# Kernel optimization log

Hardware: AMD Instinct MI355X
Metric: run time of the kernel (lower is better)

The kernel has to match this reference:

```python
import jax, jax.numpy as jnp
import numpy as np

DIM = 128
HEADS = 4
HD = DIM // HEADS  # 32
WS = 8             # search window (ws x ws candidates)
K = 16             # top-k neighbors kept
SCALE = HD ** -0.5


def _sepconv(x, w_dw, w_pw, b):
    # depthwise 3x3 ('SAME', reflect-free) + pointwise 1x1 with bias (SepConv2d)
    C = x.shape[1]
    y = jax.lax.conv_general_dilated(x, w_dw, (1, 1), 'SAME',
                                     feature_group_count=C,
                                     dimension_numbers=('NCHW', 'OIHW', 'NCHW'))
    return jnp.einsum('bchw,oc->bohw', y, w_pw) + b[None, :, None, None]


def _refl(i, n):
    # dnls reflect_bounds: mirror indices back into [0, n-1]
    i = jnp.where(i < 0, -i, i)
    return jnp.where(i >= n, 2 * (n - 1) - i, i)


def _neighbor_idx(T, H, W, ws):
    # flat pixel index of the ws*ws spatial candidates per query (wt=0: same frame)
    off = jnp.arange(ws) - ws // 2
    ni = _refl(jnp.arange(H)[:, None] + off[None, :], H)  # [H,ws]
    nj = _refl(jnp.arange(W)[:, None] + off[None, :], W)  # [W,ws]
    pix = ni[:, None, :, None] * W + nj[None, :, None, :]  # [H,W,ws,ws]
    idx = jnp.arange(T)[:, None, None, None, None] * (H * W) + pix[None]
    return idx.reshape(T * H * W, ws * ws).astype(jnp.int32)  # [Q,L]


def reference(vid, wq_dw, wq_pw, bq, wk_dw, wk_pw, bk, wv_dw, wv_pw, bv, proj_w, proj_b):
    B, T, C, H, W = vid.shape
    Q = T * H * W
    x = vid.reshape(B * T, C, H, W)
    # qkv conv projection; q pre-scaled as in get_qkv
    q = _sepconv(x, wq_dw, wq_pw, bq) * SCALE
    k = _sepconv(x, wk_dw, wk_pw, bk)
    v = _sepconv(x, wv_dw, wv_pw, bv)

    def heads(z):  # [B*T,C,H,W] -> [B,heads,Q,hd]
        return z.reshape(B, T, HEADS, HD, H, W).transpose(0, 2, 1, 4, 5, 3).reshape(B, HEADS, Q, HD)

    qh, kh, vh = heads(q), heads(k), heads(v)
    idx = _neighbor_idx(T, H, W, WS)            # [Q,L]
    kg = jnp.take(kh, idx, axis=2)              # [B,h,Q,L,hd] irregular gather
    dists = jnp.einsum('bhqd,bhqld->bhql', qh, kg)
    vals, args = jax.lax.top_k(dists, K)        # k-NN by prod distance
    attn = jax.nn.softmax(vals, axis=-1)        # run_softmax over k
    sel = jnp.take_along_axis(jnp.broadcast_to(idx[None, None], (B, HEADS) + idx.shape), args, axis=-1)
    vsel = jnp.take_along_axis(vh, sel.reshape(B, HEADS, Q * K)[..., None], axis=2).reshape(B, HEADS, Q, K, HD)
    out = jnp.einsum('bhqk,bhqkd->bhqd', attn, vsel)   # wpsum (ps=pt=1)
    out = out.transpose(0, 2, 1, 3).reshape(B, Q, C)   # merge heads: (h c)
    y = out @ proj_w.T + proj_b                        # nn.Linear proj
    # fold: ps=1, stride0=1 -> zvid==1, pure reshape back to video
    return y.reshape(B, T, H, W, C).transpose(0, 1, 4, 2, 3)


def setup_inputs() -> dict:
    key = jax.random.key(0)
    ks = jax.random.split(key, 12)
    s = 0.02
    return {
        'vid': jax.random.normal(ks[0], (1, 2, DIM, 96, 96), jnp.float32),
        'wq_dw': jax.random.normal(ks[1], (DIM, 1, 3, 3), jnp.float32) * s,
        'wq_pw': jax.random.normal(ks[2], (DIM, DIM), jnp.float32) * s,
        'bq': jax.random.normal(ks[3], (DIM,), jnp.float32) * s,
        'wk_dw': jax.random.normal(ks[4], (DIM, 1, 3, 3), jnp.float32) * s,
        'wk_pw': jax.random.normal(ks[5], (DIM, DIM), jnp.float32) * s,
        'bk': jax.random.normal(ks[6], (DIM,), jnp.float32) * s,
        'wv_dw': jax.random.normal(ks[7], (DIM, 1, 3, 3), jnp.float32) * s,
        'wv_pw': jax.random.normal(ks[8], (DIM, DIM), jnp.float32) * s,
        'bv': jax.random.normal(ks[9], (DIM,), jnp.float32) * s,
        'proj_w': jax.random.normal(ks[10], (DIM, DIM), jnp.float32) * s,
        'proj_b': jax.random.normal(ks[11], (DIM,), jnp.float32) * s,
    }
```

## Files before the change

### kernel.cpp

```cpp
#include <hip/hip_runtime.h>
#include <math.h>

#define TT 2
#define CH 128
#define HH 96
#define WW 96
#define HWS 9216
#define QTOT 18432
#define QC (QTOT*CH)
#define HD 32
#define KTOP 16
#define SCALE 0.17677669529663687f

#define SEG 16
#define PR 8
#define PC 23
#define PSTRIDE 36

#define FPX 32

#define WB_TOT 98304

typedef __attribute__((ext_vector_type(8))) short short8;
typedef __attribute__((ext_vector_type(4))) float floatx4;

__device__ __forceinline__ unsigned short f2bf(float f) {
    union { float f; unsigned u; } x; x.f = f;
    unsigned r = x.u + 0x7fffu + ((x.u >> 16) & 1u);
    return (unsigned short)(r >> 16);
}
__device__ __forceinline__ float bf2f(unsigned short h) {
    return __uint_as_float(((unsigned)h) << 16);
}

__device__ __forceinline__ int refl(int x, int n) {
    x = x < 0 ? -x : x;
    return x >= n ? 2 * (n - 1) - x : x;
}

__global__ __launch_bounds__(256) void wprep_kernel(
    const float* __restrict__ wq_pw, const float* __restrict__ wk_pw,
    const float* __restrict__ wv_pw, const float* __restrict__ proj_w,
    unsigned short* __restrict__ wbuf)
{
    int t = threadIdx.x;
    int y = blockIdx.x;
    const float* src = y == 0 ? wq_pw : (y == 1 ? wk_pw : (y == 2 ? wv_pw : proj_w));
    unsigned short* hi = wbuf + (y == 0 ? 0 : (y == 1 ? 32768 : (y == 2 ? 65536 : 81920)));
#pragma unroll
    for (int r = 0; r < 16; r++) {
        int idx = r * 256 + t;
        float4 w4 = *(const float4*)(src + idx * 4);
        unsigned short hx = f2bf(w4.x), hy = f2bf(w4.y), hz = f2bf(w4.z), hw = f2bf(w4.w);
        uint2 pk;
        pk.x = hx | ((unsigned)hy << 16); pk.y = hz | ((unsigned)hw << 16);
        *(uint2*)(hi + idx * 4) = pk;
        if (y < 2) {
            unsigned short lx = f2bf(w4.x - bf2f(hx)), ly = f2bf(w4.y - bf2f(hy));
            unsigned short lz = f2bf(w4.z - bf2f(hz)), lw = f2bf(w4.w - bf2f(hw));
            pk.x = lx | ((unsigned)ly << 16); pk.y = lz | ((unsigned)lw << 16);
            *(uint2*)(hi + 16384 + idx * 4) = pk;
        }
    }
}

__global__ __launch_bounds__(512) void dwqkv_kernel(
    const float* __restrict__ x,
    const float* __restrict__ wqd, const float* __restrict__ wkd, const float* __restrict__ wvd,
    const unsigned short* __restrict__ wbuf,
    const float* __restrict__ bq, const float* __restrict__ bk, const float* __restrict__ bv,
    float* __restrict__ qkf,
    unsigned short* __restrict__ vh)
{
    __shared__ float wS[3456];
    __shared__ unsigned short pl[5][FPX * 136];
    int t = threadIdx.x;
    for (int r = t; r < 1152; r += 512) {
        wS[r] = wqd[r]; wS[1152 + r] = wkd[r]; wS[2304 + r] = wvd[r];
    }
    int p0 = blockIdx.x * FPX;
    int tt0 = p0 / HWS;
    int hw0 = p0 - tt0 * HWS;
    int i0 = hw0 / WW, j0 = hw0 - i0 * WW;
    int px = t & 31, cgp = t >> 5;
    int c0 = cgp * 8;
    int j = j0 + px;

    int off[9]; float mk[9];
#pragma unroll
    for (int r = 0; r < 3; r++) {
        int ii = i0 + r - 1;
        float rm = (ii >= 0 && ii < HH) ? 1.f : 0.f;
        int iic = ii < 0 ? 0 : (ii >= HH ? HH - 1 : ii);
#pragma unroll
        for (int s = 0; s < 3; s++) {
            int jj = j + s - 1;
            float cm = (jj >= 0 && jj < WW) ? 1.f : 0.f;
            int jjc = jj < 0 ? 0 : (jj >= WW ? WW - 1 : jj);
            off[r * 3 + s] = iic * WW + jjc;
            mk[r * 3 + s] = rm * cm;
        }
    }
    __syncthreads();

    unsigned qh[4], ql2[4], kh[4], kl[4], vh4[4];
#pragma unroll
    for (int ic = 0; ic < 8; ic += 2) {
        float sv[3][2];
#pragma unroll
        for (int u = 0; u < 2; u++) {
            int c = c0 + ic + u;
            const float* xp = x + (size_t)(tt0 * CH + c) * HWS;
            const float* w0 = &wS[c * 9];
            const float* w1 = &wS[1152 + c * 9];
            const float* w2 = &wS[2304 + c * 9];
            float s0 = 0.f, s1 = 0.f, s2 = 0.f;
#pragma unroll
            for (int q9 = 0; q9 < 9; q9++) {
                float xv = xp[off[q9]] * mk[q9];
                s0 += xv * w0[q9]; s1 += xv * w1[q9]; s2 += xv * w2[q9];
            }
            sv[0][u] = s0; sv[1][u] = s1; sv[2][u] = s2;
        }
        int w = ic >> 1;
        unsigned short h0 = f2bf(sv[0][0]), h1 = f2bf(sv[0][1]);
        qh[w] = h0 | ((unsigned)h1 << 16);
        ql2[w] = f2bf(sv[0][0] - bf2f(h0)) | ((unsigned)f2bf(sv[0][1] - bf2f(h1)) << 16);
        h0 = f2bf(sv[1][0]); h1 = f2bf(sv[1][1]);
        kh[w] = h0 | ((unsigned)h1 << 16);
        kl[w] = f2bf(sv[1][0] - bf2f(h0)) | ((unsigned)f2bf(sv[1][1] - bf2f(h1)) << 16);
        vh4[w] = f2bf(sv[2][0]) | ((unsigned)f2bf(sv[2][1]) << 16);
    }
    int lb = px * 136 + c0;
    uint4 pk;
    pk.x = qh[0];  pk.y = qh[1];  pk.z = qh[2];  pk.w = qh[3];  *(uint4*)&pl[0][lb] = pk;
    pk.x = ql2[0]; pk.y = ql2[1]; pk.z = ql2[2]; pk.w = ql2[3]; *(uint4*)&pl[1][lb] = pk;
    pk.x = kh[0];  pk.y = kh[1];  pk.z = kh[2];  pk.w = kh[3];  *(uint4*)&pl[2][lb] = pk;
    pk.x = kl[0];  pk.y = kl[1];  pk.z = kl[2];  pk.w = kl[3];  *(uint4*)&pl[3][lb] = pk;
    pk.x = vh4[0]; pk.y = vh4[1]; pk.z = vh4[2]; pk.w = vh4[3]; *(uint4*)&pl[4][lb] = pk;
    __syncthreads();

    int wv = t >> 6, lane = t & 63;
    int m = lane & 15, quad = lane >> 4;
    int o0 = (wv & 3) * 32;
    bool isQ = wv < 4;
    const unsigned short* Wh_g = wbuf + (isQ ? 0 : 32768);
    const unsigned short* Wl_g = Wh_g + 16384;
    const unsigned short* Ah = pl[isQ ? 0 : 2];
    const unsigned short* Al = pl[isQ ? 1 : 3];
    const float* bias = isQ ? bq : bk;
    float scale = isQ ? SCALE : 1.f;
    float* O = qkf + (isQ ? 0 : (size_t)QC);
    float bb[2];
#pragma unroll
    for (int ot = 0; ot < 2; ot++) bb[ot] = bias[o0 + ot * 16 + m];
    floatx4 acc[2][2];
#pragma unroll
    for (int i = 0; i < 2; i++)
#pragma unroll
        for (int jj2 = 0; jj2 < 2; jj2++) acc[i][jj2] = (floatx4){0.f, 0.f, 0.f, 0.f};
#pragma unroll
    for (int kc = 0; kc < 4; kc++) {
        short8 avh[2], avl[2], bh2[2], bl2[2];
#pragma unroll
        for (int pt = 0; pt < 2; pt++) {
            int lidx = (pt * 16 + m) * 136 + kc * 32 + quad * 8;
            avh[pt] = *(const short8*)&Ah[lidx];
            avl[pt] = *(const short8*)&Al[lidx];
        }
#pragma unroll
        for (int ot = 0; ot < 2; ot++) {
            size_t widx = (size_t)(o0 + ot * 16 + m) * CH + kc * 32 + quad * 8;
            bh2[ot] = *(const short8*)(Wh_g + widx);
            bl2[ot] = *(const short8*)(Wl_g + widx);
        }
#pragma unroll
        for (int pt = 0; pt < 2; pt++)
#pragma unroll
            for (int ot = 0; ot < 2; ot++) {
                acc[pt][ot] = __builtin_amdgcn_mfma_f32_16x16x32_bf16(avh[pt], bh2[ot], acc[pt][ot], 0, 0, 0);
                acc[pt][ot] = __builtin_amdgcn_mfma_f32_16x16x32_bf16(avh[pt], bl2[ot], acc[pt][ot], 0, 0, 0);
                acc[pt][ot] = __builtin_amdgcn_mfma_f32_16x16x32_bf16(avl[pt], bh2[ot], acc[pt][ot], 0, 0, 0);
            }
    }
#pragma unroll
    for (int pt = 0; pt < 2; pt++)
#pragma unroll
        for (int ot = 0; ot < 2; ot++)
#pragma unroll
            for (int reg = 0; reg < 4; reg++) {
                int p = p0 + pt * 16 + quad * 4 + reg;
                O[(size_t)p * CH + o0 + ot * 16 + m] = (acc[pt][ot][reg] + bb[ot]) * scale;
            }

    const unsigned short* Wv_g = wbuf + 65536;
    int ptv = wv >> 2;
    float bbv[2];
#pragma unroll
    for (int ot = 0; ot < 2; ot++) bbv[ot] = bv[o0 + ot * 16 + m];
    floatx4 accv[2];
    accv[0] = (floatx4){0.f, 0.f, 0.f, 0.f};
    accv[1] = (floatx4){0.f, 0.f, 0.f, 0.f};
#pragma unroll
    for (int kc = 0; kc < 4; kc++) {
        int lidx = (ptv * 16 + m) * 136 + kc * 32 + quad * 8;
        short8 av = *(const short8*)&pl[4][lidx];
#pragma unroll
        for (int ot = 0; ot < 2; ot++) {
            size_t widx = (size_t)(o0 + ot * 16 + m) * CH + kc * 32 + quad * 8;
            short8 bhv = *(const short8*)(Wv_g + widx);
            accv[ot] = __builtin_amdgcn_mfma_f32_16x16x32_bf16(av, bhv, accv[ot], 0, 0, 0);
        }
    }
    unsigned short* vhh = vh + (size_t)(wv & 3) * QTOT * 32;
#pragma unroll
    for (int ot = 0; ot < 2; ot++)
#pragma unroll
        for (int reg = 0; reg < 4; reg++) {
            int p = p0 + ptv * 16 + quad * 4 + reg;
            vhh[(size_t)p * 32 + ot * 16 + m] = f2bf(accv[ot][reg] + bbv[ot]);
        }
}

__global__ __launch_bounds__(1024) void attn_kernel(
    const float* __restrict__ q,
    const float* __restrict__ k,
    const unsigned short* __restrict__ vh,
    unsigned short* __restrict__ att)
{
    __shared__ float kp[PR * PC * PSTRIDE];
    __shared__ uint2 slot[16][KTOP];
    int h = blockIdx.y;
    int n = blockIdx.x;
    int seg = (n & 7) * 144 + (n >> 3);
    int qj0 = (seg % (WW / SEG)) * SEG;
    int qi = (seg / (WW / SEG)) % HH;
    int tt = seg / ((WW / SEG) * HH);
    int t = threadIdx.x;

#pragma unroll
    for (int r = 0; r < 2; r++) {
        int f = r * 1024 + t;
        if (f < PR * PC * 8) {
            int pix = f >> 3, d4 = f & 7;
            int ci = pix / PC, cj = pix - ci * PC;
            int gi = refl(qi + ci - 4, HH);
            int gj = refl(qj0 + cj - 4, WW);
            int gp = tt * HWS + gi * WW + gj;
            *(float4*)(&kp[pix * PSTRIDE + d4 * 4]) =
                *(const float4*)(k + (size_t)gp * CH + h * HD + d4 * 4);
        }
    }

    int wv = t >> 6, lane = t & 63;
    int wvu = __builtin_amdgcn_readfirstlane(wv);
    if (lane < KTOP) slot[wvu][lane] = make_uint2(0u, 0u);
    __syncthreads();

    int ci = lane >> 3, cjo = lane & 7;
    int di = ci - 4, dj = cjo - 4;
    int rowoff = tt * HWS + refl(qi + di, HH) * WW;
    const unsigned long long below = (1ull << lane) - 1ull;
    const unsigned short* vhh = vh + (size_t)h * QTOT * 32;

    int ql = wvu;
    int qj = qj0 + ql;
    int p = tt * HWS + qi * WW + qj;

    const float* qp = q + (size_t)p * CH + h * HD;
    int pixq = ci * PC + ql + cjo;
    const float* kr = &kp[pixq * PSTRIDE];
    float dist = 0.f;
#pragma unroll
    for (int dd = 0; dd < 8; dd++) {
        float4 qv = *(const float4*)(qp + dd * 4);
        float4 kv = *(const float4*)(kr + dd * 4);
        dist += qv.x * kv.x + qv.y * kv.y + qv.z * kv.z + qv.w * kv.w;
    }

    unsigned u = __float_as_uint(dist);
    unsigned key = (u & 0x80000000u) ? ~u : (u | 0x80000000u);
    unsigned khi = key >> 16, klo = key & 0xffffu;
    float e = __expf(dist);

    unsigned Lh = 0u;
#pragma unroll
    for (int bit = 15; bit >= 0; --bit) {
        unsigned C = Lh | (1u << bit);
        unsigned long long b = __ballot(khi >= C);
        Lh = (__popcll(b) >= KTOP) ? C : Lh;
    }
    bool gth = khi > Lh;
    bool eqh = (khi == Lh);
    unsigned long long gtmh = __ballot(gth);
    unsigned long long eqmh = __ballot(eqh);
    int need = KTOP - __popcll(gtmh);
    bool selb;
    unsigned long long selm;
    if (__popcll(eqmh) == need) {
        selb = gth || eqh;
        selm = gtmh | eqmh;
    } else {
        unsigned Ll = 0u;
#pragma unroll
        for (int bit = 15; bit >= 0; --bit) {
            unsigned C = Ll | (1u << bit);
            unsigned long long b = __ballot(klo >= C) & eqmh;
            Ll = (__popcll(b) >= need) ? C : Ll;
        }
        unsigned long long gtml = __ballot(klo > Ll) & eqmh;
        unsigned long long eqml = __ballot(klo == Ll) & eqmh;
        int needl = need - __popcll(gtml);
        int rk = __popcll(eqml & below);
        bool gtl = eqh && (klo > Ll);
        bool eql = eqh && (klo == Ll);
        selb = gth || gtl || (eql && rk < needl);
        selm = __ballot(selb);
    }
    int rksel = __builtin_amdgcn_mbcnt_hi(
        (unsigned)(selm >> 32), __builtin_amdgcn_mbcnt_lo((unsigned)selm, 0));
    int cpix = rowoff + refl(qj + dj, WW);
    if (selb && rksel < KTOP)
        slot[wvu][rksel] = make_uint2(__float_as_uint(e), (unsigned)(cpix << 5));

    const int d = lane & (HD - 1);
    const int half8 = (lane >> 5) * 8;
    float acc = 0.f, denom = 0.f;
#pragma unroll
    for (int r = 0; r < 8; r++) {
        uint2 sp = slot[wvu][half8 + r];
        float a0 = __uint_as_float(sp.x);
        denom += a0;
        acc += a0 * bf2f(vhh[(size_t)sp.y + d]);
    }
    acc += __shfl_xor(acc, 32);
    denom += __shfl_xor(denom, 32);
    if (lane < HD)
        att[(size_t)p * CH + h * HD + lane] =
            f2bf(acc * __builtin_amdgcn_rcpf(denom));
}

__global__ __launch_bounds__(256) void proj_mfma(
    const unsigned short* __restrict__ A,
    const unsigned short* __restrict__ wbuf,
    const float* __restrict__ bias,
    float* __restrict__ out)
{
    const unsigned short* Wg = wbuf + 81920;
    int t = threadIdx.x;
    int wv = t >> 6, lane = t & 63;
    int m = lane & 15, quad = lane >> 4;
    int p0 = blockIdx.x * 64;
    int o0 = wv * 32;
    float bb[2][4];
#pragma unroll
    for (int ot = 0; ot < 2; ot++)
#pragma unroll
        for (int reg = 0; reg < 4; reg++) bb[ot][reg] = bias[o0 + ot * 16 + quad * 4 + reg];
    floatx4 acc[2][4];
#pragma unroll
    for (int i = 0; i < 2; i++)
#pragma unroll
        for (int jj2 = 0; jj2 < 4; jj2++) acc[i][jj2] = (floatx4){0.f, 0.f, 0.f, 0.f};
#pragma unroll
    for (int kc = 0; kc < 4; kc++) {
        short8 a[2], b[4];
#pragma unroll
        for (int ot = 0; ot < 2; ot++)
            a[ot] = *(const short8*)(Wg + (size_t)(o0 + ot * 16 + m) * CH + kc * 32 + quad * 8);
#pragma unroll
        for (int pt = 0; pt < 4; pt++)
            b[pt] = *(const short8*)(A + (size_t)(p0 + pt * 16 + m) * CH + kc * 32 + quad * 8);
#pragma unroll
        for (int ot = 0; ot < 2; ot++)
#pragma unroll
            for (int pt = 0; pt < 4; pt++)
                acc[ot][pt] = __builtin_amdgcn_mfma_f32_16x16x32_bf16(a[ot], b[pt], acc[ot][pt], 0, 0, 0);
    }
    int tt = p0 / HWS;
    int hwb = p0 - tt * HWS;
#pragma unroll
    for (int ot = 0; ot < 2; ot++)
#pragma unroll
        for (int pt = 0; pt < 4; pt++)
#pragma unroll
            for (int reg = 0; reg < 4; reg++) {
                int o = o0 + ot * 16 + quad * 4 + reg;
                int hw = hwb + pt * 16 + m;
                out[((size_t)(tt * CH + o)) * HWS + hw] = acc[ot][pt][reg] + bb[ot][reg];
            }
}

extern "C" void kernel_launch(void* const* d_in, const int* in_sizes, int n_in,
                              void* d_out, int out_size, void* d_ws, size_t ws_size,
                              hipStream_t stream) {
    const float* vid    = (const float*)d_in[0];
    const float* wq_dw  = (const float*)d_in[1];
    const float* wq_pw  = (const float*)d_in[2];
    const float* bq     = (const float*)d_in[3];
    const float* wk_dw  = (const float*)d_in[4];
    const float* wk_pw  = (const float*)d_in[5];
    const float* bk     = (const float*)d_in[6];
    const float* wv_dw  = (const float*)d_in[7];
    const float* wv_pw  = (const float*)d_in[8];
    const float* bv     = (const float*)d_in[9];
    const float* proj_w = (const float*)d_in[10];
    const float* proj_b = (const float*)d_in[11];
    float* out = (float*)d_out;

    float* qkf = (float*)d_ws;
    unsigned short* vh = (unsigned short*)(qkf + (size_t)2 * QC);
    unsigned short* att_bf = vh + (size_t)QC;
    unsigned short* wbuf = att_bf + (size_t)QC;

    wprep_kernel<<<4, 256, 0, stream>>>(wq_pw, wk_pw, wv_pw, proj_w, wbuf);
    dwqkv_kernel<<<QTOT / FPX, 512, 0, stream>>>(
        vid, wq_dw, wk_dw, wv_dw, wbuf, bq, bk, bv, qkf, vh);
    attn_kernel<<<dim3(TT * HH * (WW / SEG), 4), 1024, 0, stream>>>(
        qkf, qkf + (size_t)QC, vh, att_bf);
    proj_mfma<<<QTOT / 64, 256, 0, stream>>>(att_bf, wbuf, proj_b, out);
}
```

Measured before the change: 167.8 us.

## Compute attention distances with split-bf16 MFMA over shared key patch

Replaces the per-lane fp32 dot product between each query and its window of keys with a block-level matrix multiply. The 16 queries and the 184-pixel key patch are split into bf16 hi/lo parts, and three bf16 MFMAs emulate near-fp32 precision. Results go to a shared distance table that each lane then reads. This removes redundant per-lane global q loads and scalar FMAs, at the cost of extra conversion work, more shared memory and an additional barrier. It computes all 16x192 pairs, although each query only needs 64 of them.

```diff
diff --git a/kernel.cpp b/kernel.cpp
--- a/kernel.cpp
+++ b/kernel.cpp
@@ -15,7 +15,6 @@
 #define SEG 16
 #define PR 8
 #define PC 23
-#define PSTRIDE 36
 
 #define FPX 32
 
@@ -228,7 +227,11 @@
     const unsigned short* __restrict__ vh,
     unsigned short* __restrict__ att)
 {
-    __shared__ float kp[PR * PC * PSTRIDE];
+    __shared__ unsigned short kph[192 * 36];
+    __shared__ unsigned short kpl[192 * 36];
+    __shared__ unsigned short qsh[16 * 40];
+    __shared__ unsigned short qsl[16 * 40];
+    __shared__ float distT[16 * 196];
     __shared__ uint2 slot[16][KTOP];
     int h = blockIdx.y;
     int n = blockIdx.x;
@@ -241,20 +244,52 @@
 #pragma unroll
     for (int r = 0; r < 2; r++) {
         int f = r * 1024 + t;
-        if (f < PR * PC * 8) {
+        if (f < 192 * 8) {
             int pix = f >> 3, d4 = f & 7;
-            int ci = pix / PC, cj = pix - ci * PC;
+            int spix = pix < PR * PC ? pix : PR * PC - 1;
+            int ci = spix / PC, cj = spix - ci * PC;
             int gi = refl(qi + ci - 4, HH);
             int gj = refl(qj0 + cj - 4, WW);
             int gp = tt * HWS + gi * WW + gj;
-            *(float4*)(&kp[pix * PSTRIDE + d4 * 4]) =
-                *(const float4*)(k + (size_t)gp * CH + h * HD + d4 * 4);
-        }
-    }
-
+            float4 kv = *(const float4*)(k + (size_t)gp * CH + h * HD + d4 * 4);
+            unsigned short h0 = f2bf(kv.x), h1 = f2bf(kv.y), h2 = f2bf(kv.z), h3 = f2bf(kv.w);
+            uint2 ph;
+            ph.x = h0 | ((unsigned)h1 << 16); ph.y = h2 | ((unsigned)h3 << 16);
+            *(uint2*)&kph[pix * 36 + d4 * 4] = ph;
+            uint2 plo;
+            plo.x = f2bf(kv.x - bf2f(h0)) | ((unsigned)f2bf(kv.y - bf2f(h1)) << 16);
+            plo.y = f2bf(kv.z - bf2f(h2)) | ((unsigned)f2bf(kv.w - bf2f(h3)) << 16);
+            *(uint2*)&kpl[pix * 36 + d4 * 4] = plo;
+        }
+    }
+    if (t < 512) {
+        int qq = t >> 5, ch = t & 31;
+        int p = tt * HWS + qi * WW + qj0 + qq;
+        float qv = q[(size_t)p * CH + h * HD + ch];
+        unsigned short qhi = f2bf(qv);
+        qsh[qq * 40 + ch] = qhi;
+        qsl[qq * 40 + ch] = f2bf(qv - bf2f(qhi));
+    }
     int wv = t >> 6, lane = t & 63;
     int wvu = __builtin_amdgcn_readfirstlane(wv);
     if (lane < KTOP) slot[wvu][lane] = make_uint2(0u, 0u);
+    __syncthreads();
+
+    int m = lane & 15, quad = lane >> 4;
+    if (wvu < 12) {
+        short8 ah = *(const short8*)&qsh[m * 40 + quad * 8];
+        short8 al = *(const short8*)&qsl[m * 40 + quad * 8];
+        int krow = wvu * 16 + m;
+        short8 bh = *(const short8*)&kph[krow * 36 + quad * 8];
+        short8 bl = *(const short8*)&kpl[krow * 36 + quad * 8];
+        floatx4 dacc = (floatx4){0.f, 0.f, 0.f, 0.f};
+        dacc = __builtin_amdgcn_mfma_f32_16x16x32_bf16(ah, bh, dacc, 0, 0, 0);
+        dacc = __builtin_amdgcn_mfma_f32_16x16x32_bf16(ah, bl, dacc, 0, 0, 0);
+        dacc = __builtin_amdgcn_mfma_f32_16x16x32_bf16(al, bh, dacc, 0, 0, 0);
+#pragma unroll
+        for (int reg = 0; reg < 4; reg++)
+            distT[(quad * 4 + reg) * 196 + wvu * 16 + m] = dacc[reg];
+    }
     __syncthreads();
 
     int ci = lane >> 3, cjo = lane & 7;
@@ -266,17 +301,8 @@
     int ql = wvu;
     int qj = qj0 + ql;
     int p = tt * HWS + qi * WW + qj;
-
-    const float* qp = q + (size_t)p * CH + h * HD;
     int pixq = ci * PC + ql + cjo;
-    const float* kr = &kp[pixq * PSTRIDE];
-    float dist = 0.f;
-#pragma unroll
-    for (int dd = 0; dd < 8; dd++) {
-        float4 qv = *(const float4*)(qp + dd * 4);
-        float4 kv = *(const float4*)(kr + dd * 4);
-        dist += qv.x * kv.x + qv.y * kv.y + qv.z * kv.z + qv.w * kv.w;
-    }
+    float dist = distT[wvu * 196 + pixq];
 
     unsigned u = __float_as_uint(dist);
     unsigned key = (u & 0x80000000u) ? ~u : (u | 0x80000000u);
```

Result: slower. 171.5 us (+2.3%).
